# Performance work log

Measured on AMD Instinct MI355X. Metric: run time of the kernel, lower is better.

## Reference

```python
import jax, jax.numpy as jnp
import numpy as np

TOKEN_NUM = 81   # init default token_num
KNN_K = 2        # hardcoded in apply_clustering
LAYER_INDEX = 3


def setup_inputs() -> dict:
    key = jax.random.key(0)
    k1, k2, k3 = jax.random.split(key, 3)
    B, F, N, C = 8, 1024, 17, 512
    x = jax.random.normal(k1, (B, F, N, C), dtype=jnp.float32)
    # nn.Parameter init normal_(std=0.02)
    pos_embed_token = 0.02 * jax.random.normal(k2, (1, TOKEN_NUM, C), dtype=jnp.float32)
    # deterministic stand-in for torch.rand tie-breaker noise on density
    density_noise = jax.random.uniform(k3, (B, F), dtype=jnp.float32)
    return {"x": x, "pos_embed_token": pos_embed_token,
            "density_noise": density_noise, "current_layer": LAYER_INDEX}


def _dpc_knn_index(x_knn, density_noise, cluster_num, k):
    # x_knn: (B, F, C) pooled features; returns sorted cluster-center indices (B, cluster_num)
    B, F, C = x_knn.shape
    sq = jnp.sum(x_knn * x_knn, axis=-1)                       # (B, F)
    d2 = sq[:, :, None] + sq[:, None, :] - 2.0 * jnp.einsum('bic,bjc->bij', x_knn, x_knn)
    dist = jnp.sqrt(jnp.maximum(d2, 0.0)) / jnp.sqrt(jnp.asarray(C, x_knn.dtype))  # cdist / C**0.5
    # k smallest distances (self included, dist 0)
    neg_nearest, _ = jax.lax.top_k(-dist, k)                   # (B, F, k)
    dist_nearest = -neg_nearest
    density = jnp.exp(-jnp.mean(dist_nearest ** 2, axis=-1))   # (B, F)
    density = density + density_noise * 1e-6                   # tie-breaker
    # mask[b,i,j] = density[b,j] > density[b,i]
    mask = (density[:, None, :] > density[:, :, None]).astype(x_knn.dtype)
    dist_max = jnp.max(dist.reshape(B, -1), axis=-1)[:, None, None]
    min_dist = jnp.min(dist * mask + dist_max * (1.0 - mask), axis=-1)  # (B, F)
    score = min_dist * density
    _, index_down = jax.lax.top_k(score, cluster_num)          # (B, cluster_num)
    return jnp.sort(index_down, axis=-1)


def reference(x, pos_embed_token, density_noise, current_layer):
    # forward path only hits clustering when current_layer == layer_index
    if current_layer != LAYER_INDEX:
        return x
    B, F, N, C = x.shape
    # AdaptiveAvgPool1d(1) over joint axis after 'b f n c -> b (f c) n' == mean over n
    x_knn = jnp.mean(x, axis=2)                                # (B, F, C)
    index = _dpc_knn_index(x_knn, density_noise, TOKEN_NUM, KNN_K)
    index = jax.lax.stop_gradient(index)                       # clustering is under no_grad
    # gather selected frames: x[batch, index] -> (B, token_num, N, C)
    compressed = jnp.take_along_axis(x, index[:, :, None, None], axis=1)
    # '+ pos_embed_token' applied per (b n) f c  ==  broadcast over joints
    compressed = compressed + pos_embed_token[:, :, None, :]
    return compressed
```

## Files before the change

kernel.cpp:

```cpp
#include <hip/hip_runtime.h>
#include <math.h>
#include <float.h>

#define BB 8
#define FF 1024
#define NJ 17
#define CH 512
#define TOK 81
#define TS 128
#define BK 16
#define SQRT_C 22.627416997969522f

__global__ __launch_bounds__(128) void pool_kernel(const float* __restrict__ x,
                                                   float* __restrict__ xknn,
                                                   float* __restrict__ sq) {
    const int row = blockIdx.x;
    const int t = threadIdx.x;
    const float* px = x + (size_t)row * NJ * CH + t * 4;
    float4 acc = make_float4(0.f, 0.f, 0.f, 0.f);
    #pragma unroll
    for (int n = 0; n < NJ; ++n) {
        const float4 v = *(const float4*)(px + (size_t)n * CH);
        acc.x += v.x; acc.y += v.y; acc.z += v.z; acc.w += v.w;
    }
    acc.x /= 17.0f; acc.y /= 17.0f; acc.z /= 17.0f; acc.w /= 17.0f;
    *(float4*)(xknn + (size_t)row * CH + t * 4) = acc;
    float s = acc.x * acc.x + acc.y * acc.y + acc.z * acc.z + acc.w * acc.w;
    #pragma unroll
    for (int off = 32; off > 0; off >>= 1) s += __shfl_down(s, off);
    __shared__ float wsum[2];
    if ((t & 63) == 0) wsum[t >> 6] = s;
    __syncthreads();
    if (t == 0) sq[row] = wsum[0] + wsum[1];
}

__device__ inline void merge2(float& lo0, float& lo1, float c0, float c1) {
    float n0 = fminf(lo0, c0);
    float n1 = fminf(fmaxf(lo0, c0), fminf(lo1, c1));
    lo0 = n0; lo1 = n1;
}

__global__ __launch_bounds__(256) void passA_kernel(const float* __restrict__ xknn,
                                                    const float* __restrict__ sq,
                                                    float* __restrict__ dist) {
    const int ct = blockIdx.x, rt = blockIdx.y, b = blockIdx.z;
    const int tid = threadIdx.x;
    const int tx = tid & 15, ty = tid >> 4;
    __shared__ float As[BK][132];
    __shared__ float Bs[BK][132];

    const float* Ab = xknn + ((size_t)b * FF + rt * TS) * CH;
    const float* Bb = xknn + ((size_t)b * FF + ct * TS) * CH;
    const int lrow = tid >> 1;
    const int lk   = (tid & 1) * 8;

    float4 a0 = *(const float4*)(Ab + (size_t)lrow * CH + lk);
    float4 a1 = *(const float4*)(Ab + (size_t)lrow * CH + lk + 4);
    float4 b0 = *(const float4*)(Bb + (size_t)lrow * CH + lk);
    float4 b1 = *(const float4*)(Bb + (size_t)lrow * CH + lk + 4);

    float acc[8][8] = {};
    for (int kt = 0; kt < CH; kt += BK) {
        __syncthreads();
        As[lk + 0][lrow] = a0.x; As[lk + 1][lrow] = a0.y;
        As[lk + 2][lrow] = a0.z; As[lk + 3][lrow] = a0.w;
        As[lk + 4][lrow] = a1.x; As[lk + 5][lrow] = a1.y;
        As[lk + 6][lrow] = a1.z; As[lk + 7][lrow] = a1.w;
        Bs[lk + 0][lrow] = b0.x; Bs[lk + 1][lrow] = b0.y;
        Bs[lk + 2][lrow] = b0.z; Bs[lk + 3][lrow] = b0.w;
        Bs[lk + 4][lrow] = b1.x; Bs[lk + 5][lrow] = b1.y;
        Bs[lk + 6][lrow] = b1.z; Bs[lk + 7][lrow] = b1.w;
        __syncthreads();
        if (kt + BK < CH) {
            const int ko = kt + BK + lk;
            a0 = *(const float4*)(Ab + (size_t)lrow * CH + ko);
            a1 = *(const float4*)(Ab + (size_t)lrow * CH + ko + 4);
            b0 = *(const float4*)(Bb + (size_t)lrow * CH + ko);
            b1 = *(const float4*)(Bb + (size_t)lrow * CH + ko + 4);
        }
        #pragma unroll
        for (int kk = 0; kk < BK; ++kk) {
            const float4 av0 = *(const float4*)&As[kk][ty * 8];
            const float4 av1 = *(const float4*)&As[kk][ty * 8 + 4];
            const float4 bv0 = *(const float4*)&Bs[kk][tx * 8];
            const float4 bv1 = *(const float4*)&Bs[kk][tx * 8 + 4];
            const float am[8] = {av0.x, av0.y, av0.z, av0.w, av1.x, av1.y, av1.z, av1.w};
            const float bn[8] = {bv0.x, bv0.y, bv0.z, bv0.w, bv1.x, bv1.y, bv1.z, bv1.w};
            #pragma unroll
            for (int m = 0; m < 8; ++m)
                #pragma unroll
                for (int n = 0; n < 8; ++n)
                    acc[m][n] = fmaf(am[m], bn[n], acc[m][n]);
        }
    }

    const int row0 = rt * TS + ty * 8;
    const int col0 = ct * TS + tx * 8;
    float sqb[8];
    #pragma unroll
    for (int n = 0; n < 8; ++n) sqb[n] = sq[b * FF + col0 + n];
    #pragma unroll
    for (int m = 0; m < 8; ++m) {
        const float sa = sq[b * FF + row0 + m];
        float d[8];
        #pragma unroll
        for (int n = 0; n < 8; ++n) {
            float d2 = sa + sqb[n] - 2.0f * acc[m][n];
            d[n] = sqrtf(fmaxf(d2, 0.0f)) / SQRT_C;
        }
        float* dst = dist + ((size_t)b * FF + row0 + m) * FF + col0;
        *(float4*)(dst)     = make_float4(d[0], d[1], d[2], d[3]);
        *(float4*)(dst + 4) = make_float4(d[4], d[5], d[6], d[7]);
    }
}

__global__ __launch_bounds__(256) void rowstat_kernel(const float* __restrict__ dist,
                                                      const float* __restrict__ noise,
                                                      float* __restrict__ density,
                                                      float* __restrict__ rowmax) {
    const int r = blockIdx.x * 4 + (threadIdx.x >> 6);
    const int lane = threadIdx.x & 63;
    const float* dr = dist + (size_t)r * FF;
    float lo0 = FLT_MAX, lo1 = FLT_MAX, mx = -FLT_MAX;
    #pragma unroll
    for (int j = 0; j < FF / 64; ++j) {
        const float d = dr[lane + j * 64];
        mx = fmaxf(mx, d);
        merge2(lo0, lo1, d, FLT_MAX);
    }
    #pragma unroll
    for (int off = 32; off > 0; off >>= 1) {
        const float o0 = __shfl_down(lo0, off);
        const float o1 = __shfl_down(lo1, off);
        const float om = __shfl_down(mx, off);
        merge2(lo0, lo1, o0, o1);
        mx = fmaxf(mx, om);
    }
    if (lane == 0) {
        density[r] = expf(-0.5f * (lo0 * lo0 + lo1 * lo1)) + noise[r] * 1e-6f;
        rowmax[r] = mx;
    }
}

__global__ __launch_bounds__(256) void batchmax_kernel(const float* __restrict__ rowmax,
                                                       float* __restrict__ distmax) {
    const int b = blockIdx.x, t = threadIdx.x;
    float mx = -FLT_MAX;
    for (int j = t; j < FF; j += 256) mx = fmaxf(mx, rowmax[b * FF + j]);
    #pragma unroll
    for (int off = 32; off > 0; off >>= 1) mx = fmaxf(mx, __shfl_down(mx, off));
    __shared__ float w[4];
    if ((t & 63) == 0) w[t >> 6] = mx;
    __syncthreads();
    if (t == 0) distmax[b] = fmaxf(fmaxf(w[0], w[1]), fmaxf(w[2], w[3]));
}

__global__ __launch_bounds__(256) void scoremin_kernel(const float* __restrict__ dist,
                                                       const float* __restrict__ density,
                                                       const float* __restrict__ distmax,
                                                       float* __restrict__ score) {
    const int r = blockIdx.x * 4 + (threadIdx.x >> 6);
    const int lane = threadIdx.x & 63;
    const int b = r >> 10;
    const float* dr = dist + (size_t)r * FF;
    const float* db = density + (size_t)b * FF;
    const float dme = density[r];
    float mn = FLT_MAX;
    #pragma unroll
    for (int j = 0; j < FF / 64; ++j) {
        const int c = lane + j * 64;
        const float d = dr[c];
        const float dj = db[c];
        if (dj > dme) mn = fminf(mn, d);
    }
    #pragma unroll
    for (int off = 32; off > 0; off >>= 1) mn = fminf(mn, __shfl_down(mn, off));
    if (lane == 0) {
        if (mn == FLT_MAX) mn = distmax[b];
        score[r] = mn * dme;
    }
}

__global__ __launch_bounds__(64) void topk_kernel(const float* __restrict__ score,
                                                  int* __restrict__ selsort) {
    const int b = blockIdx.x, lane = threadIdx.x;
    float s[16];
    const float* sb = score + b * FF;
    #pragma unroll
    for (int j = 0; j < 16; ++j) s[j] = sb[lane * 16 + j];
    __shared__ int sel[TOK];
    for (int it = 0; it < TOK; ++it) {
        float best = -FLT_MAX; int bi = 0;
        #pragma unroll
        for (int j = 0; j < 16; ++j) {
            if (s[j] > best) { best = s[j]; bi = lane * 16 + j; }
        }
        #pragma unroll
        for (int off = 1; off < 64; off <<= 1) {
            float ob = __shfl_xor(best, off);
            int oi = __shfl_xor(bi, off);
            if (ob > best || (ob == best && oi < bi)) { best = ob; bi = oi; }
        }
        if ((bi >> 4) == lane) s[bi & 15] = -FLT_MAX;
        if (lane == 0) sel[it] = bi;
    }
    __syncthreads();
    for (int t = lane; t < TOK; t += 64) {
        const int v = sel[t];
        int rank = 0;
        for (int j = 0; j < TOK; ++j) rank += (sel[j] < v);
        selsort[b * TOK + rank] = v;
    }
}

__global__ __launch_bounds__(256) void gather_kernel(const float* __restrict__ x,
                                                     const float* __restrict__ pos,
                                                     const int* __restrict__ selsort,
                                                     float* __restrict__ out) {
    const size_t i = (size_t)blockIdx.x * 256 + threadIdx.x;
    const size_t total = (size_t)BB * TOK * NJ * (CH / 4);
    if (i >= total) return;
    const int c4 = (int)(i & (CH / 4 - 1));
    size_t r = i >> 7;
    const int n = (int)(r % NJ); r /= NJ;
    const int t = (int)(r % TOK);
    const int b = (int)(r / TOK);
    const int f = selsort[b * TOK + t];
    float4 v = *(const float4*)(x + (((size_t)(b * FF + f)) * NJ + n) * CH + c4 * 4);
    const float4 p = *(const float4*)(pos + (size_t)t * CH + c4 * 4);
    v.x += p.x; v.y += p.y; v.z += p.z; v.w += p.w;
    *(float4*)(out + i * 4) = v;
}

extern "C" void kernel_launch(void* const* d_in, const int* in_sizes, int n_in,
                              void* d_out, int out_size, void* d_ws, size_t ws_size,
                              hipStream_t stream) {
    const float* x     = (const float*)d_in[0];
    const float* pos   = (const float*)d_in[1];
    const float* noise = (const float*)d_in[2];
    float* out = (float*)d_out;

    float* xknn    = (float*)d_ws;
    float* dist    = xknn + (size_t)BB * FF * CH;
    float* sq      = dist + (size_t)BB * FF * FF;
    float* density = sq + BB * FF;
    float* rowmax  = density + BB * FF;
    float* distmax = rowmax + BB * FF;
    float* score   = distmax + 8;
    int*   selsort = (int*)(score + BB * FF);

    pool_kernel<<<BB * FF, 128, 0, stream>>>(x, xknn, sq);
    dim3 g(FF / TS, FF / TS, BB);
    passA_kernel<<<g, 256, 0, stream>>>(xknn, sq, dist);
    rowstat_kernel<<<(BB * FF) / 4, 256, 0, stream>>>(dist, noise, density, rowmax);
    batchmax_kernel<<<BB, 256, 0, stream>>>(rowmax, distmax);
    scoremin_kernel<<<(BB * FF) / 4, 256, 0, stream>>>(dist, density, distmax, score);
    topk_kernel<<<BB, 64, 0, stream>>>(score, selsort);
    const int gtot = (int)(((size_t)BB * TOK * NJ * (CH / 4) + 255) / 256);
    gather_kernel<<<gtot, 256, 0, stream>>>(x, pos, selsort, out);
}
```

Baseline: 594.7 us.

## Compute pairwise distances with split-bf16 MFMA on upper-triangular tiles

The pooling kernel now emits the pooled features as bf16 hi/lo pairs in an MFMA-friendly interleaved layout. The FP32 SIMT GEMM is replaced with 32x32x16 bf16 MFMAs using three products (hi*hi, hi*lo, lo*hi), which approximates FP32 accuracy. Only upper-triangular tile pairs are computed, and each result is mirrored through LDS into both halves of the distance matrix. This cuts the GEMM compute roughly in half and moves it onto matrix cores. The risks are a small precision loss that could flip near-tied top-k selections, and only 36x8 blocks, which may underfill the GPU.

```diff
diff --git a/kernel.cpp b/kernel.cpp
--- a/kernel.cpp
+++ b/kernel.cpp
@@ -7,111 +7,184 @@
 #define NJ 17
 #define CH 512
 #define TOK 81
-#define TS 128
-#define BK 16
-#define SQRT_C 22.627416997969522f
-
-__global__ __launch_bounds__(128) void pool_kernel(const float* __restrict__ x,
-                                                   float* __restrict__ xknn,
+#define RCP_SQRT_C 0.04419417382415922f
+#define LP 133
+
+typedef short bf16x8 __attribute__((ext_vector_type(8)));
+typedef float f32x16 __attribute__((ext_vector_type(16)));
+
+static __device__ inline unsigned short f2bf(float f) {
+    __bf16 h = (__bf16)f;
+    return __builtin_bit_cast(unsigned short, h);
+}
+static __device__ inline float bf2f(unsigned short u) {
+    return (float)__builtin_bit_cast(__bf16, u);
+}
+
+
+__global__ __launch_bounds__(256) void pool_kernel(const float* __restrict__ x,
+                                                   uint4* __restrict__ fhi,
+                                                   uint4* __restrict__ flo,
                                                    float* __restrict__ sq) {
-    const int row = blockIdx.x;
     const int t = threadIdx.x;
-    const float* px = x + (size_t)row * NJ * CH + t * 4;
-    float4 acc = make_float4(0.f, 0.f, 0.f, 0.f);
+    const int wid = t >> 6, lane = t & 63;
+    const int row0 = blockIdx.x * 4;
+    const int row = row0 + wid;
+    const int b = row >> 10, f0 = row0 & 1023;
+    const float* px = x + (size_t)row * NJ * CH + lane * 8;
+    float a[8] = {};
     #pragma unroll
     for (int n = 0; n < NJ; ++n) {
-        const float4 v = *(const float4*)(px + (size_t)n * CH);
-        acc.x += v.x; acc.y += v.y; acc.z += v.z; acc.w += v.w;
-    }
-    acc.x /= 17.0f; acc.y /= 17.0f; acc.z /= 17.0f; acc.w /= 17.0f;
-    *(float4*)(xknn + (size_t)row * CH + t * 4) = acc;
-    float s = acc.x * acc.x + acc.y * acc.y + acc.z * acc.z + acc.w * acc.w;
-    #pragma unroll
-    for (int off = 32; off > 0; off >>= 1) s += __shfl_down(s, off);
-    __shared__ float wsum[2];
-    if ((t & 63) == 0) wsum[t >> 6] = s;
+        const float4 v0 = *(const float4*)(px + (size_t)n * CH);
+        const float4 v1 = *(const float4*)(px + (size_t)n * CH + 4);
+        a[0] += v0.x; a[1] += v0.y; a[2] += v0.z; a[3] += v0.w;
+        a[4] += v1.x; a[5] += v1.y; a[6] += v1.z; a[7] += v1.w;
+    }
+    float ssq = 0.f;
+    unsigned short hi[8], lo[8];
+    #pragma unroll
+    for (int j = 0; j < 8; ++j) {
+        const float m = a[j] / 17.0f;
+        ssq += m * m;
+        hi[j] = f2bf(m);
+        lo[j] = f2bf(m - bf2f(hi[j]));
+    }
+    #pragma unroll
+    for (int off = 32; off > 0; off >>= 1) ssq += __shfl_down(ssq, off);
+    if (lane == 0) sq[row] = ssq;
+
+    uint4 uh, ul;
+    uh.x = (unsigned)hi[0] | ((unsigned)hi[1] << 16);
+    uh.y = (unsigned)hi[2] | ((unsigned)hi[3] << 16);
+    uh.z = (unsigned)hi[4] | ((unsigned)hi[5] << 16);
+    uh.w = (unsigned)hi[6] | ((unsigned)hi[7] << 16);
+    ul.x = (unsigned)lo[0] | ((unsigned)lo[1] << 16);
+    ul.y = (unsigned)lo[2] | ((unsigned)lo[3] << 16);
+    ul.z = (unsigned)lo[4] | ((unsigned)lo[5] << 16);
+    ul.w = (unsigned)lo[6] | ((unsigned)lo[7] << 16);
+    __shared__ uint4 sh_hi[256], sh_lo[256];
+    sh_hi[lane * 4 + wid] = uh;
+    sh_lo[lane * 4 + wid] = ul;
     __syncthreads();
-    if (t == 0) sq[row] = wsum[0] + wsum[1];
+    const int k8 = t >> 2, fpr = t & 3;
+    const int s = k8 >> 1, h = k8 & 1;
+    const size_t o = (((size_t)b * 32 + s) * 2 + h) * 1024 + f0 + fpr;
+    fhi[o] = sh_hi[t];
+    flo[o] = sh_lo[t];
+}
+
+__global__ __launch_bounds__(256) void dist_kernel(const uint4* __restrict__ fhi,
+                                                   const uint4* __restrict__ flo,
+                                                   const float* __restrict__ sq,
+                                                   float* __restrict__ dist) {
+    int tri = blockIdx.x, rt = 0;
+    while (tri >= 8 - rt) { tri -= 8 - rt; ++rt; }
+    const int ct = rt + tri;
+    const bool diag = (rt == ct);
+    const int b = blockIdx.z;
+    const int tid = threadIdx.x;
+    const int w = tid >> 6, lane = tid & 63;
+    const int R = rt * 128 + (w & 1) * 64;
+    const int C = ct * 128 + (w >> 1) * 64;
+    const int h = lane >> 5, fr = lane & 31;
+
+    size_t a0 = ((size_t)b * 64 + h) * 1024 + R + fr;
+    size_t b0 = ((size_t)b * 64 + h) * 1024 + C + fr;
+
+    f32x16 acc00, acc01, acc10, acc11;
+    #pragma unroll
+    for (int i = 0; i < 16; ++i) { acc00[i] = 0.f; acc01[i] = 0.f; acc10[i] = 0.f; acc11[i] = 0.f; }
+
+    bf16x8 A0h = *(const bf16x8*)(fhi + a0), A1h = *(const bf16x8*)(fhi + a0 + 32);
+    bf16x8 A0l = *(const bf16x8*)(flo + a0), A1l = *(const bf16x8*)(flo + a0 + 32);
+    bf16x8 B0h = *(const bf16x8*)(fhi + b0), B1h = *(const bf16x8*)(fhi + b0 + 32);
+    bf16x8 B0l = *(const bf16x8*)(flo + b0), B1l = *(const bf16x8*)(flo + b0 + 32);
+
+    #pragma unroll 4
+    for (int s = 0; s < 32; ++s) {
+        const bf16x8 cA0h = A0h, cA1h = A1h, cA0l = A0l, cA1l = A1l;
+        const bf16x8 cB0h = B0h, cB1h = B1h, cB0l = B0l, cB1l = B1l;
+        if (s < 31) {
+            a0 += 2048; b0 += 2048;
+            A0h = *(const bf16x8*)(fhi + a0); A1h = *(const bf16x8*)(fhi + a0 + 32);
+            A0l = *(const bf16x8*)(flo + a0); A1l = *(const bf16x8*)(flo + a0 + 32);
+            B0h = *(const bf16x8*)(fhi + b0); B1h = *(const bf16x8*)(fhi + b0 + 32);
+            B0l = *(const bf16x8*)(flo + b0); B1l = *(const bf16x8*)(flo + b0 + 32);
+        }
+        acc00 = __builtin_amdgcn_mfma_f32_32x32x16_bf16(cA0h, cB0h, acc00, 0, 0, 0);
+        acc01 = __builtin_amdgcn_mfma_f32_32x32x16_bf16(cA0h, cB1h, acc01, 0, 0, 0);
+        acc10 = __builtin_amdgcn_mfma_f32_32x32x16_bf16(cA1h, cB0h, acc10, 0, 0, 0);
+        acc11 = __builtin_amdgcn_mfma_f32_32x32x16_bf16(cA1h, cB1h, acc11, 0, 0, 0);
+        acc00 = __builtin_amdgcn_mfma_f32_32x32x16_bf16(cA0h, cB0l, acc00, 0, 0, 0);
+        acc01 = __builtin_amdgcn_mfma_f32_32x32x16_bf16(cA0h, cB1l, acc01, 0, 0, 0);
+        acc10 = __builtin_amdgcn_mfma_f32_32x32x16_bf16(cA1h, cB0l, acc10, 0, 0, 0);
+        acc11 = __builtin_amdgcn_mfma_f32_32x32x16_bf16(cA1h, cB1l, acc11, 0, 0, 0);
+        acc00 = __builtin_amdgcn_mfma_f32_32x32x16_bf16(cA0l, cB0h, acc00, 0, 0, 0);
+        acc01 = __builtin_amdgcn_mfma_f32_32x32x16_bf16(cA0l, cB1h, acc01, 0, 0, 0);
+        acc10 = __builtin_amdgcn_mfma_f32_32x32x16_bf16(cA1l, cB0h, acc10, 0, 0, 0);
+        acc11 = __builtin_amdgcn_mfma_f32_32x32x16_bf16(cA1l, cB1h, acc11, 0, 0, 0);
+    }
+
+    __shared__ float lds[64 * LP];
+    const int bF = b * FF;
+    const int R0 = rt * 128, C0 = ct * 128;
+    const float sqc0 = sq[bF + C + fr], sqc1 = sq[bF + C + fr + 32];
+    const int lcb = (w >> 1) * 64 + fr;
+
+    #pragma unroll
+    for (int p = 0; p < 2; ++p) {
+        if ((w & 1) == p) {
+            #pragma unroll
+            for (int reg = 0; reg < 16; ++reg) {
+                const int rp = 4 * h + (reg & 3) + 8 * (reg >> 2);
+                const float sqr0 = sq[bF + R + rp];
+                const float sqr1 = sq[bF + R + rp + 32];
+                lds[rp * LP + lcb] =
+                    sqrtf(fmaxf(sqr0 + sqc0 - 2.0f * acc00[reg], 0.f)) * RCP_SQRT_C;
+                lds[rp * LP + lcb + 32] =
+                    sqrtf(fmaxf(sqr0 + sqc1 - 2.0f * acc01[reg], 0.f)) * RCP_SQRT_C;
+                lds[(rp + 32) * LP + lcb] =
+                    sqrtf(fmaxf(sqr1 + sqc0 - 2.0f * acc10[reg], 0.f)) * RCP_SQRT_C;
+                lds[(rp + 32) * LP + lcb + 32] =
+                    sqrtf(fmaxf(sqr1 + sqc1 - 2.0f * acc11[reg], 0.f)) * RCP_SQRT_C;
+            }
+        }
+        __syncthreads();
+        if (!diag) {
+            for (int q = tid; q < 64 * 128; q += 256) {
+                const int lr = q >> 7, c = q & 127;
+                dist[((size_t)bF + R0 + p * 64 + lr) * FF + C0 + c] = lds[lr * LP + c];
+            }
+            for (int q = tid; q < 64 * 128; q += 256) {
+                const int lr = q & 63, c = q >> 6;
+                dist[((size_t)bF + C0 + c) * FF + R0 + p * 64 + lr] = lds[lr * LP + c];
+            }
+        } else if (p == 0) {
+            for (int q = tid; q < 64 * 128; q += 256) {
+                const int i = q >> 7, j = q & 127;
+                const float v = (i == j) ? 0.f : (i < j ? lds[i * LP + j] : lds[j * LP + i]);
+                dist[((size_t)bF + R0 + i) * FF + C0 + j] = v;
+            }
+            for (int q = tid; q < 64 * 64; q += 256) {
+                const int i = 64 + (q >> 6), j = q & 63;
+                dist[((size_t)bF + R0 + i) * FF + C0 + j] = lds[j * LP + i];
+            }
+        } else {
+            for (int q = tid; q < 64 * 64; q += 256) {
+                const int i = 64 + (q >> 6), j = 64 + (q & 63);
+                const float v = (i == j) ? 0.f
+                               : (i < j ? lds[(i - 64) * LP + j] : lds[(j - 64) * LP + i]);
+                dist[((size_t)bF + R0 + i) * FF + C0 + j] = v;
+            }
+        }
+        __syncthreads();
+    }
 }
 
 __device__ inline void merge2(float& lo0, float& lo1, float c0, float c1) {
     float n0 = fminf(lo0, c0);
     float n1 = fminf(fmaxf(lo0, c0), fminf(lo1, c1));
     lo0 = n0; lo1 = n1;
-}
-
-__global__ __launch_bounds__(256) void passA_kernel(const float* __restrict__ xknn,
-                                                    const float* __restrict__ sq,
-                                                    float* __restrict__ dist) {
-    const int ct = blockIdx.x, rt = blockIdx.y, b = blockIdx.z;
-    const int tid = threadIdx.x;
-    const int tx = tid & 15, ty = tid >> 4;
-    __shared__ float As[BK][132];
-    __shared__ float Bs[BK][132];
-
-    const float* Ab = xknn + ((size_t)b * FF + rt * TS) * CH;
-    const float* Bb = xknn + ((size_t)b * FF + ct * TS) * CH;
-    const int lrow = tid >> 1;
-    const int lk   = (tid & 1) * 8;
-
-    float4 a0 = *(const float4*)(Ab + (size_t)lrow * CH + lk);
-    float4 a1 = *(const float4*)(Ab + (size_t)lrow * CH + lk + 4);
-    float4 b0 = *(const float4*)(Bb + (size_t)lrow * CH + lk);
-    float4 b1 = *(const float4*)(Bb + (size_t)lrow * CH + lk + 4);
-
-    float acc[8][8] = {};
-    for (int kt = 0; kt < CH; kt += BK) {
-        __syncthreads();
-        As[lk + 0][lrow] = a0.x; As[lk + 1][lrow] = a0.y;
-        As[lk + 2][lrow] = a0.z; As[lk + 3][lrow] = a0.w;
-        As[lk + 4][lrow] = a1.x; As[lk + 5][lrow] = a1.y;
-        As[lk + 6][lrow] = a1.z; As[lk + 7][lrow] = a1.w;
-        Bs[lk + 0][lrow] = b0.x; Bs[lk + 1][lrow] = b0.y;
-        Bs[lk + 2][lrow] = b0.z; Bs[lk + 3][lrow] = b0.w;
-        Bs[lk + 4][lrow] = b1.x; Bs[lk + 5][lrow] = b1.y;
-        Bs[lk + 6][lrow] = b1.z; Bs[lk + 7][lrow] = b1.w;
-        __syncthreads();
-        if (kt + BK < CH) {
-            const int ko = kt + BK + lk;
-            a0 = *(const float4*)(Ab + (size_t)lrow * CH + ko);
-            a1 = *(const float4*)(Ab + (size_t)lrow * CH + ko + 4);
-            b0 = *(const float4*)(Bb + (size_t)lrow * CH + ko);
-            b1 = *(const float4*)(Bb + (size_t)lrow * CH + ko + 4);
-        }
-        #pragma unroll
-        for (int kk = 0; kk < BK; ++kk) {
-            const float4 av0 = *(const float4*)&As[kk][ty * 8];
-            const float4 av1 = *(const float4*)&As[kk][ty * 8 + 4];
-            const float4 bv0 = *(const float4*)&Bs[kk][tx * 8];
-            const float4 bv1 = *(const float4*)&Bs[kk][tx * 8 + 4];
-            const float am[8] = {av0.x, av0.y, av0.z, av0.w, av1.x, av1.y, av1.z, av1.w};
-            const float bn[8] = {bv0.x, bv0.y, bv0.z, bv0.w, bv1.x, bv1.y, bv1.z, bv1.w};
-            #pragma unroll
-            for (int m = 0; m < 8; ++m)
-                #pragma unroll
-                for (int n = 0; n < 8; ++n)
-                    acc[m][n] = fmaf(am[m], bn[n], acc[m][n]);
-        }
-    }
-
-    const int row0 = rt * TS + ty * 8;
-    const int col0 = ct * TS + tx * 8;
-    float sqb[8];
-    #pragma unroll
-    for (int n = 0; n < 8; ++n) sqb[n] = sq[b * FF + col0 + n];
-    #pragma unroll
-    for (int m = 0; m < 8; ++m) {
-        const float sa = sq[b * FF + row0 + m];
-        float d[8];
-        #pragma unroll
-        for (int n = 0; n < 8; ++n) {
-            float d2 = sa + sqb[n] - 2.0f * acc[m][n];
-            d[n] = sqrtf(fmaxf(d2, 0.0f)) / SQRT_C;
-        }
-        float* dst = dist + ((size_t)b * FF + row0 + m) * FF + col0;
-        *(float4*)(dst)     = make_float4(d[0], d[1], d[2], d[3]);
-        *(float4*)(dst + 4) = make_float4(d[4], d[5], d[6], d[7]);
-    }
 }
 
 __global__ __launch_bounds__(256) void rowstat_kernel(const float* __restrict__ dist,
@@ -169,9 +242,7 @@
     #pragma unroll
     for (int j = 0; j < FF / 64; ++j) {
         const int c = lane + j * 64;
-        const float d = dr[c];
-        const float dj = db[c];
-        if (dj > dme) mn = fminf(mn, d);
+        if (db[c] > dme) mn = fminf(mn, dr[c]);
     }
     #pragma unroll
     for (int off = 32; off > 0; off >>= 1) mn = fminf(mn, __shfl_down(mn, off));
@@ -240,18 +311,19 @@
     const float* noise = (const float*)d_in[2];
     float* out = (float*)d_out;
 
-    float* xknn    = (float*)d_ws;
-    float* dist    = xknn + (size_t)BB * FF * CH;
-    float* sq      = dist + (size_t)BB * FF * FF;
+    uint4* fhi    = (uint4*)d_ws;
+    uint4* flo    = fhi + (size_t)BB * 32 * 2 * 1024;
+    float* dist   = (float*)(flo + (size_t)BB * 32 * 2 * 1024);
+    float* sq     = dist + (size_t)BB * FF * FF;
     float* density = sq + BB * FF;
     float* rowmax  = density + BB * FF;
     float* distmax = rowmax + BB * FF;
     float* score   = distmax + 8;
     int*   selsort = (int*)(score + BB * FF);
 
-    pool_kernel<<<BB * FF, 128, 0, stream>>>(x, xknn, sq);
-    dim3 g(FF / TS, FF / TS, BB);
-    passA_kernel<<<g, 256, 0, stream>>>(xknn, sq, dist);
+    pool_kernel<<<(BB * FF) / 4, 256, 0, stream>>>(x, fhi, flo, sq);
+    dim3 g(36, 1, BB);
+    dist_kernel<<<g, 256, 0, stream>>>(fhi, flo, sq, dist);
     rowstat_kernel<<<(BB * FF) / 4, 256, 0, stream>>>(dist, noise, density, rowmax);
     batchmax_kernel<<<BB, 256, 0, stream>>>(rowmax, distmax);
     scoremin_kernel<<<(BB * FF) / 4, 256, 0, stream>>>(dist, density, distmax, score);
```

New measurement: 527.0 us. 1.13x faster.
